# Kernel optimization log

Hardware: AMD Instinct MI355X
Metric: run time of the kernel (lower is better)

## Reference

```python
import jax, jax.numpy as jnp
import numpy as np
from jax import lax

# Surrogate spike: forward = Heaviside, backward = g / (1 + 5|x|)^2
@jax.custom_vjp
def spike_fn(x):
    return (x >= 0).astype(x.dtype)

def _spk_fwd(x):
    return spike_fn(x), x

def _spk_bwd(x, g):
    return (g / (1.0 + 5.0 * jnp.abs(x)) ** 2,)

spike_fn.defvjp(_spk_fwd, _spk_bwd)

BN_EPS = 1e-5

def _batchnorm(x, scale, bias, mean, var):
    # x: (B, C, T); eval-mode BN with running stats
    inv = scale / jnp.sqrt(var + BN_EPS)
    return x * inv[None, :, None] + (bias - mean * inv)[None, :, None]

def _conv1d(x, w, b, pad):
    y = lax.conv_general_dilated(x, w, (1,), [(pad, pad)],
                                 dimension_numbers=('NCH', 'OIH', 'NCH'))
    return y + b[None, :, None]

def setup_inputs() -> dict:
    key = jax.random.key(0)
    ks = jax.random.split(key, 12)
    B, T, EEG, GEO, TH, H, OUT = 4096, 320, 64, 18, 32, 16, 4
    inp = {
        'x_eeg': jax.random.normal(ks[0], (B, T, EEG), jnp.float32),
        'x_geo': jax.random.normal(ks[1], (B, T, GEO), jnp.float32),
        'conv1_w': jax.random.normal(ks[2], (TH, EEG, 5), jnp.float32) * 0.05,
        'conv1_b': jnp.zeros((TH,), jnp.float32),
        'bn1_s': jnp.ones((TH,), jnp.float32),
        'bn1_b': jnp.zeros((TH,), jnp.float32),
        'bn1_m': jnp.zeros((TH,), jnp.float32),
        'bn1_v': jnp.ones((TH,), jnp.float32),
        'conv2_w': jax.random.normal(ks[3], (H, TH, 3), jnp.float32) * 0.1,
        'conv2_b': jnp.zeros((H,), jnp.float32),
        'bn2_s': jnp.ones((H,), jnp.float32),
        'bn2_b': jnp.zeros((H,), jnp.float32),
        'bn2_m': jnp.zeros((H,), jnp.float32),
        'bn2_v': jnp.ones((H,), jnp.float32),
        'geo_w': jax.random.normal(ks[4], (H, GEO), jnp.float32) * 0.2,
        'geo_b': jnp.zeros((H,), jnp.float32),
        'gamma': jnp.full((H,), 0.5, jnp.float32),
        'fc1_w': jax.random.normal(ks[5], (64, 160), jnp.float32) * 0.08,
        'fc1_b': jnp.zeros((64,), jnp.float32),
        'fc2_w': jax.random.normal(ks[6], (OUT, 64), jnp.float32) * 0.12,
        'fc2_b': jnp.zeros((OUT,), jnp.float32),
    }
    return inp

def reference(x_eeg, x_geo, conv1_w, conv1_b, bn1_s, bn1_b, bn1_m, bn1_v,
              conv2_w, conv2_b, bn2_s, bn2_b, bn2_m, bn2_v,
              geo_w, geo_b, gamma, fc1_w, fc1_b, fc2_w, fc2_b):
    B, T, _ = x_eeg.shape
    theta_0, beta, tau_a, tau_m = 0.5, 1.8, 0.36, 0.8

    # EEG temporal encoder (eval mode: dropout = identity)
    h = x_eeg.transpose(0, 2, 1)  # (B, 64, T)
    h = jax.nn.relu(_batchnorm(_conv1d(h, conv1_w, conv1_b, 2), bn1_s, bn1_b, bn1_m, bn1_v))
    h = jax.nn.relu(_batchnorm(_conv1d(h, conv2_w, conv2_b, 1), bn2_s, bn2_b, bn2_m, bn2_v))
    eeg_encoded = h.transpose(0, 2, 1)  # (B, T, 16)

    geo_mod = jax.nn.sigmoid(jnp.einsum('bti,hi->bth', x_geo, geo_w) + geo_b)  # (B, T, 16)

    H = eeg_encoded.shape[-1]
    zeros = jnp.zeros((B, H), x_eeg.dtype)
    init = (zeros, zeros, zeros, zeros)  # mem_alif, eta, mem_li, prev_spk

    def step(carry, xs):
        mem_alif, eta, mem_li, prev_spk = carry
        cur_eeg, cur_geo = xs
        eta = tau_a * eta + (1.0 - tau_a) * prev_spk
        theta_t = theta_0 + beta * eta - gamma * cur_geo
        mem_alif = tau_m * mem_alif + cur_eeg
        spk = spike_fn(mem_alif - theta_t)
        mem_alif = mem_alif * (1.0 - spk)
        mem_li = 0.9 * mem_li + spk
        return (mem_alif, eta, mem_li, spk), mem_li

    xs = (eeg_encoded.transpose(1, 0, 2), geo_mod.transpose(1, 0, 2))  # (T, B, 16)
    _, pot = lax.scan(step, init, xs)  # (T, B, 16)

    pot = pot.transpose(1, 2, 0)                 # (B, 16, T)
    windows = pot.reshape(B, H, 10, 32)          # T = 320 = 10*32
    dp_feat = (windows[..., 16:].mean(-1) - windows[..., :16].mean(-1)).reshape(B, -1)  # (B, 160)

    out = jax.nn.relu(dp_feat @ fc1_w.T + fc1_b) @ fc2_w.T + fc2_b  # (B, 4)
    return out
```

## Files before the change

### kernel.cpp

```cpp
#include <hip/hip_runtime.h>
#include <math.h>

#define TB    4096
#define TSEQ  320
#define NEEG  64
#define NTH   32
#define NH    16
#define NGEO  18
#define TILE_T 48
#define NTILES 7
#define XROWS2 54
#define H1ROWS 50

typedef _Float16 f16x8 __attribute__((ext_vector_type(8)));
typedef _Float16 f16x2 __attribute__((ext_vector_type(2)));
typedef float f32x4 __attribute__((ext_vector_type(4)));
#define INV2048 4.8828125e-4f

#define OFF_W1F  0
#define OFF_W2F  10240
#define OFF_B1   11776
#define OFF_B2   11808
#define OFF_GWT  11824
#define OFF_FC1T 12112
#define OFF_FC2T 22352
#define OFF_ZP   22656
#define OFF_E    32768
#define SZ_EC    (TB*TSEQ*NH)
#define OFF_C    (OFF_E + SZ_EC)
#define OFF_DP   (OFF_C + SZ_EC)
#define SZ_DP    (TB*160)
#define REQ_FLOATS ((size_t)OFF_DP + SZ_DP)
#define REQ_BYTES  (REQ_FLOATS * 4)

__global__ void __launch_bounds__(256)
prep_kernel(const float* __restrict__ c1w, const float* __restrict__ c1b,
            const float* __restrict__ s1,  const float* __restrict__ bb1,
            const float* __restrict__ mm1, const float* __restrict__ vv1,
            const float* __restrict__ c2w, const float* __restrict__ c2b,
            const float* __restrict__ s2,  const float* __restrict__ bb2,
            const float* __restrict__ mm2, const float* __restrict__ vv2,
            const float* __restrict__ gw,  const float* __restrict__ fc1w,
            const float* __restrict__ fc2w, float* __restrict__ ws)
{
    const int tid = threadIdx.x;
    _Float16* w1fp = reinterpret_cast<_Float16*>(ws + OFF_W1F);
    _Float16* w2fp = reinterpret_cast<_Float16*>(ws + OFF_W2F);

    for (int d = tid; d < 10240; d += 256) {
        int j = d & 7, l = (d >> 3) & 63, nbk = d >> 9;
        int kk = nbk >> 1, nb = nbk & 1;
        int k = kk >> 1, i = (kk & 1) * 32 + ((l >> 4) * 8) + j;
        int c = nb * 16 + (l & 15);
        float inv = s1[c] / sqrtf(vv1[c] + 1e-5f);
        float wv = c1w[c * 320 + i * 5 + k] * inv;
        _Float16 hi = (_Float16)wv;
        _Float16 lo = (_Float16)((wv - (float)hi) * 2048.f);
        w1fp[((nbk * 2 + 0) * 64 + l) * 8 + j] = hi;
        w1fp[((nbk * 2 + 1) * 64 + l) * 8 + j] = lo;
    }
    for (int d = tid; d < 1536; d += 256) {
        int j = d & 7, l = (d >> 3) & 63, kk2 = d >> 9;
        int c = (l >> 4) * 8 + j;
        int o = l & 15;
        float inv = s2[o] / sqrtf(vv2[o] + 1e-5f);
        float wv = c2w[o * 96 + c * 3 + kk2] * inv;
        _Float16 hi = (_Float16)wv;
        _Float16 lo = (_Float16)((wv - (float)hi) * 2048.f);
        w2fp[((kk2 * 2 + 0) * 64 + l) * 8 + j] = hi;
        w2fp[((kk2 * 2 + 1) * 64 + l) * 8 + j] = lo;
    }
    if (tid < NTH) {
        float inv = s1[tid] / sqrtf(vv1[tid] + 1e-5f);
        ws[OFF_B1 + tid] = c1b[tid] * inv + bb1[tid] - mm1[tid] * inv;
    }
    if (tid < NH) {
        float inv = s2[tid] / sqrtf(vv2[tid] + 1e-5f);
        ws[OFF_B2 + tid] = c2b[tid] * inv + bb2[tid] - mm2[tid] * inv;
    }
    for (int d = tid; d < NGEO * NH; d += 256) {
        int i = d / NH, h = d - i * NH;
        ws[OFF_GWT + d] = gw[h * NGEO + i];
    }
    for (int d = tid; d < 160 * 64; d += 256) {
        int f = d / 64, o = d - f * 64;
        ws[OFF_FC1T + d] = fc1w[o * 160 + f];
    }
    if (tid < 256) {
        int j = tid / 4, o = tid - j * 4;
        ws[OFF_FC2T + tid] = fc2w[o * 64 + j];
    }
    if (tid < 64) ws[OFF_ZP + tid] = 0.f;
}

__global__ void __launch_bounds__(256, 2)
convm_kernel(const float* __restrict__ xeeg, const float* __restrict__ xgeo,
             const float* __restrict__ ws,   const float* __restrict__ geo_b,
             const float* __restrict__ gamma,
             float* __restrict__ E, float* __restrict__ C)
{
    __shared__ __align__(16) float xbuf[2][XROWS2 * 64];
    __shared__ __align__(16) float xg32[14 * 64];
    __shared__ __align__(16) _Float16 h1h[H1ROWS * 32];
    __shared__ __align__(16) _Float16 h1l[H1ROWS * 32];
    __shared__ __align__(16) float gws[NGEO * NH];
    __shared__ float b1s[32], b2s[16], gbs[16], gams[16];

    const int b = blockIdx.x, tid = threadIdx.x;
    const int l = tid & 63, w = tid >> 6;
    const int lrow = l & 15, lkg = l >> 4;
    const int nb = w >> 1, wsub = w & 1;
    const int ug = tid >> 2, hq = tid & 3;

    const float* xb  = xeeg + (size_t)b * TSEQ * NEEG;
    const float* xgb = xgeo + (size_t)b * TSEQ * NGEO;
    const float* zp  = ws + OFF_ZP;

#define STAGE_DMA(buf, t0n) do {                                                     \
        for (int c_ = w; c_ < XROWS2; c_ += 4) {                                     \
            int tg_ = (t0n) - 3 + c_;                                                \
            const float* s_ = (tg_ >= 0 && tg_ < TSEQ)                               \
                              ? (xb + (size_t)tg_ * 64 + l) : zp;                    \
            __builtin_amdgcn_global_load_lds(                                        \
                (const __attribute__((address_space(1))) void*)s_,                   \
                (__attribute__((address_space(3))) void*)&xbuf[(buf)][c_ * 64],      \
                4, 0, 0);                                                            \
        }                                                                            \
        for (int c_ = w; c_ < 14; c_ += 4) {                                         \
            int fo_ = (t0n) * NGEO + c_ * 64;                                        \
            const float* s_ = (fo_ < TSEQ * NGEO) ? (xgb + fo_ + l) : zp;            \
            __builtin_amdgcn_global_load_lds(                                        \
                (const __attribute__((address_space(1))) void*)s_,                   \
                (__attribute__((address_space(3))) void*)&xg32[c_ * 64],             \
                4, 0, 0);                                                            \
        }                                                                            \
    } while (0)

    f16x8 B1h[10], B1l[10], B2h[3], B2l[3];
    {
        const f16x8* wsrc = reinterpret_cast<const f16x8*>(ws + OFF_W1F);
        #pragma unroll
        for (int kk = 0; kk < 10; ++kk) {
            B1h[kk] = wsrc[((kk * 2 + nb) * 2 + 0) * 64 + l];
            B1l[kk] = wsrc[((kk * 2 + nb) * 2 + 1) * 64 + l];
        }
        const f16x8* wsrc2 = reinterpret_cast<const f16x8*>(ws + OFF_W2F);
        #pragma unroll
        for (int kk = 0; kk < 3; ++kk) {
            B2h[kk] = wsrc2[(kk * 2 + 0) * 64 + l];
            B2l[kk] = wsrc2[(kk * 2 + 1) * 64 + l];
        }
    }
    {
        if (tid < 32) b1s[tid] = ws[OFF_B1 + tid];
        if (tid < 16) {
            b2s[tid] = ws[OFF_B2 + tid];
            gbs[tid] = geo_b[tid];
            gams[tid] = gamma[tid];
        }
        for (int p = tid; p < NGEO * NH; p += 256) gws[p] = ws[OFF_GWT + p];
    }
    STAGE_DMA(0, 0);
    __syncthreads();

    for (int jt = 0; jt < NTILES; ++jt) {
        const int t0 = jt * TILE_T;
        const int cur = jt & 1;
        _Float16* xh = reinterpret_cast<_Float16*>(&xbuf[cur][0]);
        _Float16* xl = xh + XROWS2 * 64;

        float2 xr2[7];
        #pragma unroll
        for (int q = 0; q < 7; ++q) {
            int p = tid + q * 256;
            if (p < XROWS2 * 32) {
                int xr = p >> 5, ip = (p & 31) * 2;
                xr2[q] = *reinterpret_cast<const float2*>(&xbuf[cur][xr * 64 + ip]);
            }
        }
        if (ug < TILE_T && t0 + ug < TSEQ) {
            float z0 = gbs[hq * 4 + 0], z1 = gbs[hq * 4 + 1];
            float z2 = gbs[hq * 4 + 2], z3 = gbs[hq * 4 + 3];
            const float* xgr = &xg32[ug * NGEO];
            #pragma unroll
            for (int ii = 0; ii < NGEO; ++ii) {
                float xv = xgr[ii];
                float4 wv = *reinterpret_cast<const float4*>(&gws[ii * 16 + hq * 4]);
                z0 = fmaf(xv, wv.x, z0);
                z1 = fmaf(xv, wv.y, z1);
                z2 = fmaf(xv, wv.z, z2);
                z3 = fmaf(xv, wv.w, z3);
            }
            const int tcur = t0 + ug;
            C[((size_t)b * 16 + hq * 4 + 0) * TSEQ + tcur] = gams[hq * 4 + 0] * (1.f / (1.f + expf(-z0)));
            C[((size_t)b * 16 + hq * 4 + 1) * TSEQ + tcur] = gams[hq * 4 + 1] * (1.f / (1.f + expf(-z1)));
            C[((size_t)b * 16 + hq * 4 + 2) * TSEQ + tcur] = gams[hq * 4 + 2] * (1.f / (1.f + expf(-z2)));
            C[((size_t)b * 16 + hq * 4 + 3) * TSEQ + tcur] = gams[hq * 4 + 3] * (1.f / (1.f + expf(-z3)));
        }
        __syncthreads();

        #pragma unroll
        for (int q = 0; q < 7; ++q) {
            int p = tid + q * 256;
            if (p < XROWS2 * 32) {
                int xr = p >> 5, ip = (p & 31) * 2;
                float f0 = xr2[q].x, f1 = xr2[q].y;
                _Float16 h0 = (_Float16)f0, h1v = (_Float16)f1;
                f16x2 vh = {h0, h1v};
                f16x2 vl = {(_Float16)((f0 - (float)h0) * 2048.f),
                            (_Float16)((f1 - (float)h1v) * 2048.f)};
                int idx = xr * 64 + (((ip >> 3) ^ (xr & 7)) << 3) + (ip & 7);
                *reinterpret_cast<f16x2*>(&xh[idx]) = vh;
                *reinterpret_cast<f16x2*>(&xl[idx]) = vl;
            }
        }
        __syncthreads();

        if (jt + 1 < NTILES) STAGE_DMA(cur ^ 1, (jt + 1) * TILE_T);
        __builtin_amdgcn_s_setprio(1);
        {
            const float bia = b1s[nb * 16 + lrow];
            #pragma unroll
            for (int pi = 0; pi < 2; ++pi) {
                const int mb = wsub + pi * 2;
                const int mbase = mb * 16;
                int s = mbase + lrow; if (s > H1ROWS - 1) s = H1ROWS - 1;
                f32x4 aH = {0.f, 0.f, 0.f, 0.f};
                f32x4 aM = aH, aL = aH;
                #pragma unroll
                for (int kk = 0; kk < 10; ++kk) {
                    const int xr = s + (kk >> 1);
                    const int gx = (kk & 1) * 4 + lkg;
                    const int off = xr * 64 + ((gx ^ (xr & 7)) << 3);
                    f16x8 Ah = *reinterpret_cast<const f16x8*>(&xh[off]);
                    f16x8 Al = *reinterpret_cast<const f16x8*>(&xl[off]);
                    aH = __builtin_amdgcn_mfma_f32_16x16x32_f16(Ah, B1h[kk], aH, 0, 0, 0);
                    aM = __builtin_amdgcn_mfma_f32_16x16x32_f16(Ah, B1l[kk], aM, 0, 0, 0);
                    aL = __builtin_amdgcn_mfma_f32_16x16x32_f16(Al, B1h[kk], aL, 0, 0, 0);
                }
                #pragma unroll
                for (int r = 0; r < 4; ++r) {
                    int so = mbase + lkg * 4 + r;
                    if (so < H1ROWS) {
                        int tg = t0 - 1 + so;
                        bool v = (tg >= 0 && tg < TSEQ);
                        float val = v ? fmaxf(fmaf(aM[r] + aL[r], INV2048, aH[r]) + bia, 0.f) : 0.f;
                        int key = (so >> 1) & 3;
                        int g = (nb * 2 + (lrow >> 3)) ^ key;
                        int idx = so * 32 + (g << 3) + (lrow & 7);
                        _Float16 hh = (_Float16)val;
                        h1h[idx] = hh;
                        h1l[idx] = (_Float16)((val - (float)hh) * 2048.f);
                    }
                }
            }
        }
        __builtin_amdgcn_s_setprio(0);
        __syncthreads();

        if (w < 3 && t0 + w * 16 < TSEQ) {
            const int ub = w * 16;
            f32x4 aH = {0.f, 0.f, 0.f, 0.f};
            f32x4 aM = aH, aL = aH;
            __builtin_amdgcn_s_setprio(1);
            #pragma unroll
            for (int kk = 0; kk < 3; ++kk) {
                int srow = ub + lrow + kk;
                int off = srow * 32 + ((lkg ^ ((srow >> 1) & 3)) << 3);
                f16x8 Ah = *reinterpret_cast<const f16x8*>(&h1h[off]);
                f16x8 Al = *reinterpret_cast<const f16x8*>(&h1l[off]);
                aH = __builtin_amdgcn_mfma_f32_16x16x32_f16(Ah, B2h[kk], aH, 0, 0, 0);
                aM = __builtin_amdgcn_mfma_f32_16x16x32_f16(Ah, B2l[kk], aM, 0, 0, 0);
                aL = __builtin_amdgcn_mfma_f32_16x16x32_f16(Al, B2h[kk], aL, 0, 0, 0);
            }
            __builtin_amdgcn_s_setprio(0);
            const float bia = b2s[lrow];
            float4 ev;
            float* evp = reinterpret_cast<float*>(&ev);
            #pragma unroll
            for (int r = 0; r < 4; ++r)
                evp[r] = fmaxf(fmaf(aM[r] + aL[r], INV2048, aH[r]) + bia, 0.f);
            float* ep = E + ((size_t)b * 16 + lrow) * TSEQ + t0 + ub + lkg * 4;
            *reinterpret_cast<float4*>(ep) = ev;
        }
    }
#undef STAGE_DMA
}

__global__ void __launch_bounds__(256)
scan_kernel(const float* __restrict__ E, const float* __restrict__ C,
            float* __restrict__ DP)
{
    const int tid = threadIdx.x;
    const int h = tid & 15;
    const int b = blockIdx.x * 16 + (tid >> 4);
    const float4* e4 = reinterpret_cast<const float4*>(E) + ((size_t)b * 16 + h) * 80;
    const float4* c4 = reinterpret_cast<const float4*>(C) + ((size_t)b * 16 + h) * 80;

    float eta = 0.f, memv = 0.f, li = 0.f, ps = 0.f, accF = 0.f, accS = 0.f;
    float4 ev = e4[0], cv = c4[0];
    for (int t4 = 0; t4 < 80; ++t4) {
        float4 en, cn;
        if (t4 < 79) { en = e4[t4 + 1]; cn = c4[t4 + 1]; }
        const float* evp = reinterpret_cast<const float*>(&ev);
        const float* cvp = reinterpret_cast<const float*>(&cv);
        #pragma unroll
        for (int tt = 0; tt < 4; ++tt) {
            float e = evp[tt], c = cvp[tt];
            eta = 0.36f * eta + 0.64f * ps;
            float theta = 0.5f + 1.8f * eta - c;
            memv = 0.8f * memv + e;
            float spk = (memv - theta >= 0.f) ? 1.f : 0.f;
            memv *= (1.f - spk);
            li = 0.9f * li + spk;
            ps = spk;
            int t = t4 * 4 + tt;
            if (((t >> 4) & 1) == 0) accF += li; else accS += li;
        }
        if ((t4 & 7) == 7) {
            DP[(size_t)b * 160 + h * 10 + (t4 >> 3)] = (accS - accF) * 0.0625f;
            accF = 0.f; accS = 0.f;
        }
        ev = en; cv = cn;
    }
}

__global__ void __launch_bounds__(256)
fc_kernel(const float* __restrict__ DP, const float* __restrict__ ws,
          const float* __restrict__ fc1_b, const float* __restrict__ fc2_b,
          float* __restrict__ out)
{
    __shared__ float sh_dp[4][160];
    __shared__ float mid[4][64];
    const int tid = threadIdx.x;
    const int b0 = blockIdx.x * 4;
    for (int p = tid; p < 640; p += 256)
        sh_dp[p / 160][p - (p / 160) * 160] = DP[(size_t)b0 * 160 + p];
    __syncthreads();
    {
        const int bl = tid >> 6, o = tid & 63;
        const float* __restrict__ fc1t = ws + OFF_FC1T;
        float z = fc1_b[o];
        for (int f = 0; f < 160; ++f) z = fmaf(sh_dp[bl][f], fc1t[f * 64 + o], z);
        mid[bl][o] = fmaxf(z, 0.f);
    }
    __syncthreads();
    if (tid < 16) {
        const int bl = tid >> 2, oo = tid & 3;
        const float* __restrict__ fc2t = ws + OFF_FC2T;
        float z = fc2_b[oo];
        #pragma unroll
        for (int jj = 0; jj < 64; ++jj) z = fmaf(mid[bl][jj], fc2t[jj * 4 + oo], z);
        out[(size_t)(b0 + bl) * 4 + oo] = z;
    }
}

extern "C" void kernel_launch(void* const* d_in, const int* in_sizes, int n_in,
                              void* d_out, int out_size, void* d_ws, size_t ws_size,
                              hipStream_t stream)
{
    const float* xeeg = (const float*)d_in[0];
    const float* xgeo = (const float*)d_in[1];
    const float* c1w  = (const float*)d_in[2];
    const float* c1b  = (const float*)d_in[3];
    const float* s1   = (const float*)d_in[4];
    const float* bb1  = (const float*)d_in[5];
    const float* mm1  = (const float*)d_in[6];
    const float* vv1  = (const float*)d_in[7];
    const float* c2w  = (const float*)d_in[8];
    const float* c2b  = (const float*)d_in[9];
    const float* s2   = (const float*)d_in[10];
    const float* bb2  = (const float*)d_in[11];
    const float* mm2  = (const float*)d_in[12];
    const float* vv2  = (const float*)d_in[13];
    const float* gw   = (const float*)d_in[14];
    const float* gb   = (const float*)d_in[15];
    const float* gam  = (const float*)d_in[16];
    const float* fc1w = (const float*)d_in[17];
    const float* fc1b = (const float*)d_in[18];
    const float* fc2w = (const float*)d_in[19];
    const float* fc2b = (const float*)d_in[20];
    float* ws   = (float*)d_ws;
    float* outp = (float*)d_out;

    hipLaunchKernelGGL(prep_kernel, dim3(1), dim3(256), 0, stream,
                       c1w, c1b, s1, bb1, mm1, vv1, c2w, c2b, s2, bb2, mm2, vv2,
                       gw, fc1w, fc2w, ws);

    float* E  = ws + OFF_E;
    float* C  = ws + OFF_C;
    float* DP = ws + OFF_DP;
    hipLaunchKernelGGL(convm_kernel, dim3(TB), dim3(256), 0, stream,
                       xeeg, xgeo, ws, gb, gam, E, C);
    hipLaunchKernelGGL(scan_kernel, dim3(TB / 16), dim3(256), 0, stream,
                       E, C, DP);
    hipLaunchKernelGGL(fc_kernel, dim3(TB / 4), dim3(256), 0, stream,
                       DP, ws, fc1b, fc2b, outp);
}
```

Baseline: 334.3 us.

## Store E and C time-major in float4 slabs; move conv2 weights to LDS

The intermediate E and C tensors are rewritten in a time-major layout of [T/4][B][16][4], so the scan kernel's per-thread float4 loads at each step become contiguous across threads instead of strided by 320 floats. The producer now writes C with a 4-float stride and E with float4 stores into the new layout. Separately, the conv2 MFMA B-operands move from registers into shared memory to lower VGPR pressure, which adds LDS reads inside the conv2 loop. The producer-side C stores become scattered at a 16-byte stride.

```diff
diff --git a/kernel.cpp b/kernel.cpp
--- a/kernel.cpp
+++ b/kernel.cpp
@@ -101,6 +101,7 @@
 {
     __shared__ __align__(16) float xbuf[2][XROWS2 * 64];
     __shared__ __align__(16) float xg32[14 * 64];
+    __shared__ __align__(16) _Float16 w2f[3][2][64][8];
     __shared__ __align__(16) _Float16 h1h[H1ROWS * 32];
     __shared__ __align__(16) _Float16 h1l[H1ROWS * 32];
     __shared__ __align__(16) float gws[NGEO * NH];
@@ -136,7 +137,7 @@
         }                                                                            \
     } while (0)
 
-    f16x8 B1h[10], B1l[10], B2h[3], B2l[3];
+    f16x8 B1h[10], B1l[10];
     {
         const f16x8* wsrc = reinterpret_cast<const f16x8*>(ws + OFF_W1F);
         #pragma unroll
@@ -144,14 +145,11 @@
             B1h[kk] = wsrc[((kk * 2 + nb) * 2 + 0) * 64 + l];
             B1l[kk] = wsrc[((kk * 2 + nb) * 2 + 1) * 64 + l];
         }
-        const f16x8* wsrc2 = reinterpret_cast<const f16x8*>(ws + OFF_W2F);
-        #pragma unroll
-        for (int kk = 0; kk < 3; ++kk) {
-            B2h[kk] = wsrc2[(kk * 2 + 0) * 64 + l];
-            B2l[kk] = wsrc2[(kk * 2 + 1) * 64 + l];
-        }
     }
     {
+        const float4* s2 = reinterpret_cast<const float4*>(ws + OFF_W2F);
+        float4* d2 = reinterpret_cast<float4*>(&w2f[0][0][0][0]);
+        for (int p = tid; p < 384; p += 256) d2[p] = s2[p];
         if (tid < 32) b1s[tid] = ws[OFF_B1 + tid];
         if (tid < 16) {
             b2s[tid] = ws[OFF_B2 + tid];
@@ -191,11 +189,12 @@
                 z2 = fmaf(xv, wv.z, z2);
                 z3 = fmaf(xv, wv.w, z3);
             }
-            const int tcur = t0 + ug;
-            C[((size_t)b * 16 + hq * 4 + 0) * TSEQ + tcur] = gams[hq * 4 + 0] * (1.f / (1.f + expf(-z0)));
-            C[((size_t)b * 16 + hq * 4 + 1) * TSEQ + tcur] = gams[hq * 4 + 1] * (1.f / (1.f + expf(-z1)));
-            C[((size_t)b * 16 + hq * 4 + 2) * TSEQ + tcur] = gams[hq * 4 + 2] * (1.f / (1.f + expf(-z2)));
-            C[((size_t)b * 16 + hq * 4 + 3) * TSEQ + tcur] = gams[hq * 4 + 3] * (1.f / (1.f + expf(-z3)));
+            const int t4o = (t0 + ug) >> 2, tt = ug & 3;
+            float* cp = C + (((size_t)t4o * TB + b) * 16 + hq * 4) * 4 + tt;
+            cp[0]  = gams[hq * 4 + 0] * (1.f / (1.f + expf(-z0)));
+            cp[4]  = gams[hq * 4 + 1] * (1.f / (1.f + expf(-z1)));
+            cp[8]  = gams[hq * 4 + 2] * (1.f / (1.f + expf(-z2)));
+            cp[12] = gams[hq * 4 + 3] * (1.f / (1.f + expf(-z3)));
         }
         __syncthreads();
 
@@ -269,9 +268,11 @@
                 int off = srow * 32 + ((lkg ^ ((srow >> 1) & 3)) << 3);
                 f16x8 Ah = *reinterpret_cast<const f16x8*>(&h1h[off]);
                 f16x8 Al = *reinterpret_cast<const f16x8*>(&h1l[off]);
-                aH = __builtin_amdgcn_mfma_f32_16x16x32_f16(Ah, B2h[kk], aH, 0, 0, 0);
-                aM = __builtin_amdgcn_mfma_f32_16x16x32_f16(Ah, B2l[kk], aM, 0, 0, 0);
-                aL = __builtin_amdgcn_mfma_f32_16x16x32_f16(Al, B2h[kk], aL, 0, 0, 0);
+                f16x8 Bh = *reinterpret_cast<const f16x8*>(&w2f[kk][0][l][0]);
+                f16x8 Bl = *reinterpret_cast<const f16x8*>(&w2f[kk][1][l][0]);
+                aH = __builtin_amdgcn_mfma_f32_16x16x32_f16(Ah, Bh, aH, 0, 0, 0);
+                aM = __builtin_amdgcn_mfma_f32_16x16x32_f16(Ah, Bl, aM, 0, 0, 0);
+                aL = __builtin_amdgcn_mfma_f32_16x16x32_f16(Al, Bh, aL, 0, 0, 0);
             }
             __builtin_amdgcn_s_setprio(0);
             const float bia = b2s[lrow];
@@ -280,7 +281,8 @@
             #pragma unroll
             for (int r = 0; r < 4; ++r)
                 evp[r] = fmaxf(fmaf(aM[r] + aL[r], INV2048, aH[r]) + bia, 0.f);
-            float* ep = E + ((size_t)b * 16 + lrow) * TSEQ + t0 + ub + lkg * 4;
+            const int t4o = ((t0 + ub) >> 2) + lkg;
+            float* ep = E + (((size_t)t4o * TB + b) * 16 + lrow) * 4;
             *reinterpret_cast<float4*>(ep) = ev;
         }
     }
@@ -294,14 +296,16 @@
     const int tid = threadIdx.x;
     const int h = tid & 15;
     const int b = blockIdx.x * 16 + (tid >> 4);
-    const float4* e4 = reinterpret_cast<const float4*>(E) + ((size_t)b * 16 + h) * 80;
-    const float4* c4 = reinterpret_cast<const float4*>(C) + ((size_t)b * 16 + h) * 80;
+    const float4* e4 = reinterpret_cast<const float4*>(E);
+    const float4* c4 = reinterpret_cast<const float4*>(C);
+    const size_t idx = (size_t)b * 16 + h;
+    const size_t slab = (size_t)TB * 16;
 
     float eta = 0.f, memv = 0.f, li = 0.f, ps = 0.f, accF = 0.f, accS = 0.f;
-    float4 ev = e4[0], cv = c4[0];
+    float4 ev = e4[idx], cv = c4[idx];
     for (int t4 = 0; t4 < 80; ++t4) {
         float4 en, cn;
-        if (t4 < 79) { en = e4[t4 + 1]; cn = c4[t4 + 1]; }
+        if (t4 < 79) { en = e4[(size_t)(t4 + 1) * slab + idx]; cn = c4[(size_t)(t4 + 1) * slab + idx]; }
         const float* evp = reinterpret_cast<const float*>(&ev);
         const float* cvp = reinterpret_cast<const float*>(&cv);
         #pragma unroll
```

Result: no change. 337.0 us (+0.8%).
